# Kernel tuning notes

Hardware: AMD Instinct MI355X
Metric: run time of the kernel (lower is better)

## Reference

```python
import jax, jax.numpy as jnp
import numpy as np

B, L, S, H, C = 64, 512, 512, 768, 9  # batch, bert subword len, word seq len, hidden, num_classes


def setup_inputs() -> dict:
    key = jax.random.key(0)
    k1, k2, k3 = jax.random.split(key, 3)
    rng = np.random.RandomState(0)
    # per-word subword counts in {1,2,3}; truncate so totals fit in L subword slots
    lens = rng.randint(1, 4, size=(B, S))
    cum = lens.cumsum(axis=1)
    keep = cum <= L
    ids_lens = (lens * keep).astype(np.int32)
    totals = ids_lens.sum(axis=1)
    attention_mask = (np.arange(L)[None, :] < totals[:, None]).astype(np.int32)
    label_mask = ids_lens > 0
    label_ids = (rng.randint(0, C, size=(B, S)) * label_mask).astype(np.int32)
    bert_out = jax.random.normal(k1, (B, L, H), dtype=jnp.float32)
    W = jax.random.normal(k2, (H, C), dtype=jnp.float32) * 0.02
    b = jnp.zeros((C,), dtype=jnp.float32)
    return {
        "bert_out": bert_out,
        "W": W,
        "b": b,
        "attention_mask": jnp.asarray(attention_mask),
        "ids_lens": jnp.asarray(ids_lens),
        "label_ids": jnp.asarray(label_ids),
        "label_mask": jnp.asarray(label_mask),
    }


def reference(bert_out, W, b, attention_mask, ids_lens, label_ids, label_mask):
    Bv, Lv, Hv = bert_out.shape
    Sv = ids_lens.shape[1]
    nseg = Bv * Sv
    am = attention_mask.astype(jnp.int32)
    # subword position within each example's valid region
    sidx = jnp.cumsum(am, axis=1) - 1                       # [B, L]
    # word index for each subword: searchsorted into cumulative word lengths
    ends = jnp.cumsum(ids_lens, axis=1)                     # [B, S]
    widx = jax.vmap(lambda e, s: jnp.searchsorted(e, s, side='right'))(ends, sidx)
    seg = jnp.where(am > 0, widx + jnp.arange(Bv)[:, None] * Sv, nseg)  # pad bucket = nseg
    flat = bert_out.reshape(Bv * Lv, Hv)
    segf = seg.reshape(Bv * Lv)
    sums = jax.ops.segment_sum(flat, segf, num_segments=nseg + 1)[:nseg]
    cnts = jax.ops.segment_sum(jnp.ones((Bv * Lv,), bert_out.dtype), segf,
                               num_segments=nseg + 1)[:nseg]
    mean = sums / jnp.maximum(cnts, 1.0)[:, None]           # segment mean (split().mean(0))
    word_mask = (ids_lens > 0).reshape(nseg)
    embed = jnp.where(word_mask[:, None], mean, 0.0).reshape(Bv, Sv, Hv)  # masked_scatter
    # dropout in eval mode = identity
    logits = embed @ W + b                                  # [B, S, C]
    logp = jax.nn.log_softmax(logits, axis=-1)
    lab = jnp.clip(label_ids, 0, W.shape[1] - 1)
    nll = -jnp.take_along_axis(logp, lab[..., None].astype(jnp.int32), axis=-1)[..., 0]
    valid = label_mask.astype(bert_out.dtype)
    loss = jnp.sum(nll * valid) / jnp.maximum(jnp.sum(valid), 1.0)
    pred = jnp.argmax(logits, axis=-1)
    return loss, pred
```

## Files before the change

kernel.cpp:

```cpp
#include <hip/hip_runtime.h>

#define BB 64
#define LL 512
#define SS 512
#define HH 768
#define CC 9
#define NWORDS (BB * SS)
#define NWAVES 4
#define WPW 4
#define WBLOCKS (NWORDS / (WPW * NWAVES))
#define WTPAD 772

__global__ __launch_bounds__(512) void scan_kernel(const int* __restrict__ ids_lens,
                                                   int* __restrict__ starts,
                                                   float* __restrict__ accum) {
    __shared__ int buf[SS];
    int b = blockIdx.x, t = threadIdx.x;
    int v = ids_lens[b * SS + t];
    buf[t] = v;
    __syncthreads();
    for (int off = 1; off < SS; off <<= 1) {
        int x = (t >= off) ? buf[t - off] : 0;
        __syncthreads();
        buf[t] += x;
        __syncthreads();
    }
    starts[b * SS + t] = buf[t] - v;
    if (b == 0 && t == 0) { accum[0] = 0.0f; ((int*)accum)[1] = 0; }
}

__device__ __forceinline__ void word_load(const float* __restrict__ bert,
                                          int g, int len, int start, int hoff,
                                          float4 v[3][3]) {
    int bidx = g >> 9;
    long row0 = (long)bidx * LL + (start < LL ? start : LL - 1);
    int len1 = len > 0 ? len : 1;
    long r1 = row0 + (len1 > 1 ? 1 : 0);
    long r2 = row0 + (len1 > 2 ? 2 : 0);
    const float* p0 = bert + row0 * HH + hoff;
    const float* p1 = bert + r1 * HH + hoff;
    const float* p2 = bert + r2 * HH + hoff;
#pragma unroll
    for (int c3 = 0; c3 < 3; c3++) {
        v[0][c3] = *reinterpret_cast<const float4*>(p0 + c3 * 256);
        v[1][c3] = *reinterpret_cast<const float4*>(p1 + c3 * 256);
        v[2][c3] = *reinterpret_cast<const float4*>(p2 + c3 * 256);
    }
}

__device__ __forceinline__ void word_combine(const float4 v[3][3], int len, float m[12]) {
    float w0 = len > 0 ? 1.0f : 0.0f;
    float w1 = len > 1 ? 1.0f : 0.0f;
    float w2 = len > 2 ? 1.0f : 0.0f;
    float inv = 1.0f / (float)(len > 0 ? len : 1);
#pragma unroll
    for (int c3 = 0; c3 < 3; c3++) {
        m[c3 * 4 + 0] = (v[0][c3].x * w0 + v[1][c3].x * w1 + v[2][c3].x * w2) * inv;
        m[c3 * 4 + 1] = (v[0][c3].y * w0 + v[1][c3].y * w1 + v[2][c3].y * w2) * inv;
        m[c3 * 4 + 2] = (v[0][c3].z * w0 + v[1][c3].z * w1 + v[2][c3].z * w2) * inv;
        m[c3 * 4 + 3] = (v[0][c3].w * w0 + v[1][c3].w * w1 + v[2][c3].w * w2) * inv;
    }
}

__global__ __launch_bounds__(256) void word_kernel(
    const float* __restrict__ bert,
    const float* __restrict__ Wm,
    const float* __restrict__ bias,
    const int* __restrict__ ids_lens,
    const int* __restrict__ label_ids,
    const int* __restrict__ starts,
    float* __restrict__ pred_out,
    float* __restrict__ accum)
{
    __shared__ __align__(16) float WT[CC][WTPAD];
    __shared__ float s_nll[NWAVES];
    __shared__ int s_cnt[NWAVES];

    for (int i = threadIdx.x; i < HH * CC; i += 256) {
        int h = i / CC;
        int c = i - h * CC;
        WT[c][h] = Wm[i];
    }
    __syncthreads();

    int wave = threadIdx.x >> 6;
    int lane = threadIdx.x & 63;
    int hoff = lane * 4;

    float bs[CC];
#pragma unroll
    for (int c = 0; c < CC; c++) bs[c] = bias[c];

    float nll_acc = 0.0f;
    int cnt_acc = 0;
    int gbase = (blockIdx.x * NWAVES + wave) * WPW;

#pragma unroll
    for (int p = 0; p < WPW / 2; ++p) {
        int ga = gbase + 2 * p;
        int gb = ga + 1;
        int lena = ids_lens[ga], lenb = ids_lens[gb];
        int sta = starts[ga], stb = starts[gb];

        float4 va[3][3], vb[3][3];
        word_load(bert, ga, lena, sta, hoff, va);
        word_load(bert, gb, lenb, stb, hoff, vb);

        float ma[12], mb[12];
        word_combine(va, lena, ma);
        word_combine(vb, lenb, mb);

        float la[CC], lb[CC];
#pragma unroll
        for (int c = 0; c < CC; c++) { la[c] = 0.0f; lb[c] = 0.0f; }
#pragma unroll
        for (int c3 = 0; c3 < 3; c3++) {
#pragma unroll
            for (int c = 0; c < CC; c++) {
                float4 wv = *reinterpret_cast<const float4*>(&WT[c][c3 * 256 + hoff]);
                la[c] += ma[c3 * 4 + 0] * wv.x + ma[c3 * 4 + 1] * wv.y
                       + ma[c3 * 4 + 2] * wv.z + ma[c3 * 4 + 3] * wv.w;
                lb[c] += mb[c3 * 4 + 0] * wv.x + mb[c3 * 4 + 1] * wv.y
                       + mb[c3 * 4 + 2] * wv.z + mb[c3 * 4 + 3] * wv.w;
            }
        }

#pragma unroll
        for (int s = 0; s < 2; ++s) {
            float* lg = (s == 0) ? la : lb;
            int g = (s == 0) ? ga : gb;
            int len = (s == 0) ? lena : lenb;
#pragma unroll
            for (int c = 0; c < CC; c++) {
                float v = lg[c];
#pragma unroll
                for (int off = 32; off > 0; off >>= 1) v += __shfl_xor(v, off, 64);
                lg[c] = v + bs[c];
            }
            float mx = lg[0];
            int arg = 0;
#pragma unroll
            for (int c = 1; c < CC; c++) {
                if (lg[c] > mx) { mx = lg[c]; arg = c; }
            }
            float se = 0.0f;
#pragma unroll
            for (int c = 0; c < CC; c++) se += expf(lg[c] - mx);
            float lse = mx + logf(se);
            int lab = label_ids[g];
            lab = lab < 0 ? 0 : (lab > CC - 1 ? CC - 1 : lab);
            int valid = (len > 0) ? 1 : 0;
            nll_acc += (lse - lg[lab]) * (float)valid;
            cnt_acc += valid;
            if (lane == 0) pred_out[g] = (float)arg;
        }
    }

    if (lane == 0) { s_nll[wave] = nll_acc; s_cnt[wave] = cnt_acc; }
    __syncthreads();
    if (threadIdx.x == 0) {
        atomicAdd(accum, s_nll[0] + s_nll[1] + s_nll[2] + s_nll[3]);
        atomicAdd((int*)accum + 1, s_cnt[0] + s_cnt[1] + s_cnt[2] + s_cnt[3]);
    }
}

__global__ void finalize_kernel(const float* __restrict__ accum,
                                float* __restrict__ out_loss) {
    float s = accum[0];
    int c = ((const int*)accum)[1];
    out_loss[0] = s / fmaxf((float)c, 1.0f);
}

extern "C" void kernel_launch(void* const* d_in, const int* in_sizes, int n_in,
                              void* d_out, int out_size, void* d_ws, size_t ws_size,
                              hipStream_t stream) {
    const float* bert = (const float*)d_in[0];
    const float* Wm   = (const float*)d_in[1];
    const float* bias = (const float*)d_in[2];
    const int* ids_lens  = (const int*)d_in[4];
    const int* label_ids = (const int*)d_in[5];

    float* out = (float*)d_out;

    int*   starts = (int*)d_ws;
    float* accum  = (float*)((char*)d_ws + NWORDS * sizeof(int));

    scan_kernel<<<BB, SS, 0, stream>>>(ids_lens, starts, accum);
    word_kernel<<<WBLOCKS, 256, 0, stream>>>(bert, Wm, bias, ids_lens, label_ids,
                                             starts, out + 1, accum);
    finalize_kernel<<<1, 1, 0, stream>>>(accum, out);
}
```

Measured before the change: 197.3 us.

## Skip unused subword loads, DPP wave reductions, batch softmax per block

Each word's subword rows are now loaded only when they exist, using conditional accumulation. The old code always fetched three rows and masked them, so roughly a third of the HBM reads were padding. Cross-lane logit reductions use a DPP row/bcast sequence that leaves the sum in lane 63, which writes the logits to shared memory. One wave then does the softmax, argmax and NLL for all 64 words of the block and issues a single pair of atomics. The block grows to 8 waves × 8 words, which means fewer blocks but a larger W transpose per block, and the branchy loads may reduce memory-level parallelism.

Result: faster. 172.6 us (-12.5%).

```diff
diff --git a/kernel.cpp b/kernel.cpp
--- a/kernel.cpp
+++ b/kernel.cpp
@@ -6,10 +6,12 @@
 #define HH 768
 #define CC 9
 #define NWORDS (BB * SS)
-#define NWAVES 4
-#define WPW 4
-#define WBLOCKS (NWORDS / (WPW * NWAVES))
+#define NWAVES 8
+#define WPW 8
+#define WORDS_PER_BLOCK (NWAVES * WPW)
+#define WBLOCKS (NWORDS / WORDS_PER_BLOCK)
 #define WTPAD 772
+#define LGPAD 13
 
 __global__ __launch_bounds__(512) void scan_kernel(const int* __restrict__ ids_lens,
                                                    int* __restrict__ starts,
@@ -29,40 +31,33 @@
     if (b == 0 && t == 0) { accum[0] = 0.0f; ((int*)accum)[1] = 0; }
 }
 
-__device__ __forceinline__ void word_load(const float* __restrict__ bert,
-                                          int g, int len, int start, int hoff,
-                                          float4 v[3][3]) {
-    int bidx = g >> 9;
-    long row0 = (long)bidx * LL + (start < LL ? start : LL - 1);
-    int len1 = len > 0 ? len : 1;
-    long r1 = row0 + (len1 > 1 ? 1 : 0);
-    long r2 = row0 + (len1 > 2 ? 2 : 0);
-    const float* p0 = bert + row0 * HH + hoff;
-    const float* p1 = bert + r1 * HH + hoff;
-    const float* p2 = bert + r2 * HH + hoff;
+__device__ __forceinline__ void acc3(const float* __restrict__ p, float m[12]) {
 #pragma unroll
     for (int c3 = 0; c3 < 3; c3++) {
-        v[0][c3] = *reinterpret_cast<const float4*>(p0 + c3 * 256);
-        v[1][c3] = *reinterpret_cast<const float4*>(p1 + c3 * 256);
-        v[2][c3] = *reinterpret_cast<const float4*>(p2 + c3 * 256);
-    }
-}
-
-__device__ __forceinline__ void word_combine(const float4 v[3][3], int len, float m[12]) {
-    float w0 = len > 0 ? 1.0f : 0.0f;
-    float w1 = len > 1 ? 1.0f : 0.0f;
-    float w2 = len > 2 ? 1.0f : 0.0f;
-    float inv = 1.0f / (float)(len > 0 ? len : 1);
-#pragma unroll
-    for (int c3 = 0; c3 < 3; c3++) {
-        m[c3 * 4 + 0] = (v[0][c3].x * w0 + v[1][c3].x * w1 + v[2][c3].x * w2) * inv;
-        m[c3 * 4 + 1] = (v[0][c3].y * w0 + v[1][c3].y * w1 + v[2][c3].y * w2) * inv;
-        m[c3 * 4 + 2] = (v[0][c3].z * w0 + v[1][c3].z * w1 + v[2][c3].z * w2) * inv;
-        m[c3 * 4 + 3] = (v[0][c3].w * w0 + v[1][c3].w * w1 + v[2][c3].w * w2) * inv;
-    }
-}
-
-__global__ __launch_bounds__(256) void word_kernel(
+        float4 u = *reinterpret_cast<const float4*>(p + c3 * 256);
+        m[c3 * 4 + 0] += u.x;
+        m[c3 * 4 + 1] += u.y;
+        m[c3 * 4 + 2] += u.z;
+        m[c3 * 4 + 3] += u.w;
+    }
+}
+
+template <int CTRL>
+__device__ __forceinline__ float dpp_add(float x) {
+    int y = __builtin_amdgcn_update_dpp(0, __float_as_int(x), CTRL, 0xf, 0xf, true);
+    return x + __int_as_float(y);
+}
+__device__ __forceinline__ float rsum64(float x) {
+    x = dpp_add<0x111>(x);
+    x = dpp_add<0x112>(x);
+    x = dpp_add<0x114>(x);
+    x = dpp_add<0x118>(x);
+    x = dpp_add<0x142>(x);
+    x = dpp_add<0x143>(x);
+    return x;
+}
+
+__global__ __launch_bounds__(512) void word_kernel(
     const float* __restrict__ bert,
     const float* __restrict__ Wm,
     const float* __restrict__ bias,
@@ -73,10 +68,9 @@
     float* __restrict__ accum)
 {
     __shared__ __align__(16) float WT[CC][WTPAD];
-    __shared__ float s_nll[NWAVES];
-    __shared__ int s_cnt[NWAVES];
-
-    for (int i = threadIdx.x; i < HH * CC; i += 256) {
+    __shared__ float LG[WORDS_PER_BLOCK][LGPAD];
+
+    for (int i = threadIdx.x; i < HH * CC; i += 512) {
         int h = i / CC;
         int c = i - h * CC;
         WT[c][h] = Wm[i];
@@ -86,14 +80,9 @@
     int wave = threadIdx.x >> 6;
     int lane = threadIdx.x & 63;
     int hoff = lane * 4;
-
-    float bs[CC];
-#pragma unroll
-    for (int c = 0; c < CC; c++) bs[c] = bias[c];
-
-    float nll_acc = 0.0f;
-    int cnt_acc = 0;
-    int gbase = (blockIdx.x * NWAVES + wave) * WPW;
+    int gblock = blockIdx.x * WORDS_PER_BLOCK;
+    int bidx = gblock >> 9;
+    int gbase = gblock + wave * WPW;
 
 #pragma unroll
     for (int p = 0; p < WPW / 2; ++p) {
@@ -102,13 +91,23 @@
         int lena = ids_lens[ga], lenb = ids_lens[gb];
         int sta = starts[ga], stb = starts[gb];
 
-        float4 va[3][3], vb[3][3];
-        word_load(bert, ga, lena, sta, hoff, va);
-        word_load(bert, gb, lenb, stb, hoff, vb);
-
         float ma[12], mb[12];
-        word_combine(va, lena, ma);
-        word_combine(vb, lenb, mb);
+#pragma unroll
+        for (int i = 0; i < 12; i++) { ma[i] = 0.0f; mb[i] = 0.0f; }
+
+        const float* pa = bert + ((size_t)bidx * LL + sta) * HH + hoff;
+        const float* pb = bert + ((size_t)bidx * LL + stb) * HH + hoff;
+        if (lena > 0) acc3(pa, ma);
+        if (lena > 1) acc3(pa + HH, ma);
+        if (lena > 2) acc3(pa + 2 * HH, ma);
+        if (lenb > 0) acc3(pb, mb);
+        if (lenb > 1) acc3(pb + HH, mb);
+        if (lenb > 2) acc3(pb + 2 * HH, mb);
+
+        float inva = 1.0f / (float)(lena > 0 ? lena : 1);
+        float invb = 1.0f / (float)(lenb > 0 ? lenb : 1);
+#pragma unroll
+        for (int i = 0; i < 12; i++) { ma[i] *= inva; mb[i] *= invb; }
 
         float la[CC], lb[CC];
 #pragma unroll
@@ -126,41 +125,56 @@
         }
 
 #pragma unroll
-        for (int s = 0; s < 2; ++s) {
-            float* lg = (s == 0) ? la : lb;
-            int g = (s == 0) ? ga : gb;
-            int len = (s == 0) ? lena : lenb;
+        for (int c = 0; c < CC; c++) { la[c] = rsum64(la[c]); lb[c] = rsum64(lb[c]); }
+        int wa = wave * WPW + 2 * p;
+        if (lane == 63) {
 #pragma unroll
             for (int c = 0; c < CC; c++) {
-                float v = lg[c];
-#pragma unroll
-                for (int off = 32; off > 0; off >>= 1) v += __shfl_xor(v, off, 64);
-                lg[c] = v + bs[c];
+                LG[wa][c] = la[c];
+                LG[wa + 1][c] = lb[c];
             }
-            float mx = lg[0];
-            int arg = 0;
-#pragma unroll
-            for (int c = 1; c < CC; c++) {
-                if (lg[c] > mx) { mx = lg[c]; arg = c; }
-            }
-            float se = 0.0f;
-#pragma unroll
-            for (int c = 0; c < CC; c++) se += expf(lg[c] - mx);
-            float lse = mx + logf(se);
-            int lab = label_ids[g];
-            lab = lab < 0 ? 0 : (lab > CC - 1 ? CC - 1 : lab);
-            int valid = (len > 0) ? 1 : 0;
-            nll_acc += (lse - lg[lab]) * (float)valid;
-            cnt_acc += valid;
-            if (lane == 0) pred_out[g] = (float)arg;
-        }
-    }
-
-    if (lane == 0) { s_nll[wave] = nll_acc; s_cnt[wave] = cnt_acc; }
+        }
+    }
+
     __syncthreads();
-    if (threadIdx.x == 0) {
-        atomicAdd(accum, s_nll[0] + s_nll[1] + s_nll[2] + s_nll[3]);
-        atomicAdd((int*)accum + 1, s_cnt[0] + s_cnt[1] + s_cnt[2] + s_cnt[3]);
+
+    if (threadIdx.x < WORDS_PER_BLOCK) {
+        int w = threadIdx.x;
+        int g = gblock + w;
+        float lg[CC];
+#pragma unroll
+        for (int c = 0; c < CC; c++) lg[c] = LG[w][c] + bias[c];
+
+        float mx = lg[0];
+        int arg = 0;
+#pragma unroll
+        for (int c = 1; c < CC; c++) {
+            if (lg[c] > mx) { mx = lg[c]; arg = c; }
+        }
+        float se = 0.0f;
+#pragma unroll
+        for (int c = 0; c < CC; c++) se += expf(lg[c] - mx);
+        float lse = mx + logf(se);
+
+        int len = ids_lens[g];
+        int lab = label_ids[g];
+        lab = lab < 0 ? 0 : (lab > CC - 1 ? CC - 1 : lab);
+        int valid = (len > 0) ? 1 : 0;
+        float nll = (lse - lg[lab]) * (float)valid;
+
+        pred_out[g] = (float)arg;
+
+        float s = nll;
+        int cn = valid;
+#pragma unroll
+        for (int off = 32; off > 0; off >>= 1) {
+            s += __shfl_xor(s, off, 64);
+            cn += __shfl_xor(cn, off, 64);
+        }
+        if (w == 0) {
+            atomicAdd(accum, s);
+            atomicAdd((int*)accum + 1, cn);
+        }
     }
 }
 
@@ -186,7 +200,7 @@
     float* accum  = (float*)((char*)d_ws + NWORDS * sizeof(int));
 
     scan_kernel<<<BB, SS, 0, stream>>>(ids_lens, starts, accum);
-    word_kernel<<<WBLOCKS, 256, 0, stream>>>(bert, Wm, bias, ids_lens, label_ids,
+    word_kernel<<<WBLOCKS, 512, 0, stream>>>(bert, Wm, bias, ids_lens, label_ids,
                                              starts, out + 1, accum);
     finalize_kernel<<<1, 1, 0, stream>>>(accum, out);
 }
```
